# Kernel tuning notes

Measured on AMD Instinct MI355X. Metric: run time of the kernel, lower is better.

## Reference

```python
import jax, jax.numpy as jnp
import numpy as np


def setup_inputs() -> dict:
    key = jax.random.key(0)
    kq, kk, kv = jax.random.split(key, 3)
    B, S, D = 32, 2048, 64
    q = jax.random.normal(kq, (B, S, D), dtype=jnp.float32)
    k = jax.random.normal(kk, (B, S, D), dtype=jnp.float32)
    v = jax.random.normal(kv, (B, S, D), dtype=jnp.float32)
    return {"q": q, "k": k, "v": v}


def reference(q, k, v):
    # attention = q @ k^T  -> [B, S, S]; scale=None, attn_mask=None path
    scores = jnp.einsum("bqd,bkd->bqk", q, k)
    attention = jax.nn.softmax(scores, axis=-1)  # softmax over dim=2 (last)
    # dropout p=0.0 -> identity
    context = jnp.einsum("bqk,bkd->bqd", attention, v) + q  # residual add
    return (context, attention)
```

## Files before the change

### kernel.cpp

```cpp
#include <hip/hip_runtime.h>

namespace {

constexpr int kB = 32;
constexpr int kS = 2048;
constexpr int kD = 64;
constexpr int BQ = 128;
constexpr int BK = 64;
constexpr int LW = 72;
constexpr int NT = kS / BK;
constexpr int NP = NT / 2;
constexpr int KSZ = BK * LW;
constexpr float kLog2e = 1.44269504088896340736f;

typedef _Float16 f16x8 __attribute__((ext_vector_type(8)));
typedef _Float16 f16x4 __attribute__((ext_vector_type(4)));
typedef float f32x4 __attribute__((ext_vector_type(4)));

#define MFMA16F(a, b, c) __builtin_amdgcn_mfma_f32_16x16x32_f16(a, b, c, 0, 0, 0)

#define LBAR()                                                  \
    do {                                                        \
        asm volatile("s_waitcnt lgkmcnt(0)" ::: "memory");      \
        __builtin_amdgcn_s_barrier();                           \
        asm volatile("" ::: "memory");                          \
    } while (0)

__global__ __launch_bounds__(512, 4)
void sdpa_kernel(const float* __restrict__ qg, const float* __restrict__ kg,
                 const float* __restrict__ vg, float* __restrict__ out) {
    __shared__ _Float16 smem[4 * KSZ + 8 * 16 * LW];
    _Float16* sP = smem + 4 * KSZ;
    _Float16* sQ = smem;

    const int tid = threadIdx.x;
    const int lane = tid & 63;
    const int g = lane >> 4;
    const int c = lane & 15;
    const int wq = tid >> 6;
    const int wrow0 = wq * 16;

    const int id = blockIdx.x;
    const int lin = (id & 7) * 64 + (id >> 3);
    const int b = lin >> 4;
    const int q0 = (lin & 15) * BQ;

    float* ctx = out;
    float* att = out + (size_t)kB * kS * kD;
    const size_t inb = (size_t)b * kS * kD;
    const float* kbase = kg + inb;

    const int srow = tid >> 4;
    const int scol = (tid & 15) * 4;

    const int vd = lane;
    const int j0v = wq * 8;

    f32x4 kr[2][2];
    #pragma unroll
    for (int t = 0; t < 2; ++t)
        #pragma unroll
        for (int i = 0; i < 2; ++i)
            kr[t][i] = *reinterpret_cast<const f32x4*>(
                kbase + (size_t)(t * BK + i * 32 + srow) * kD + scol);

    #pragma unroll
    for (int i = 0; i < 4; ++i) {
        const int row = i * 32 + srow;
        f32x4 qv = *reinterpret_cast<const f32x4*>(qg + inb + (size_t)(q0 + row) * kD + scol);
        f16x4 hv;
        #pragma unroll
        for (int e = 0; e < 4; ++e) hv[e] = (_Float16)(qv[e] * kLog2e);
        *reinterpret_cast<f16x4*>(&sQ[row * LW + scol]) = hv;
    }
    LBAR();
    f16x8 aQ0 = *reinterpret_cast<const f16x8*>(&sQ[(wrow0 + c) * LW + 8 * g]);
    f16x8 aQ1 = *reinterpret_cast<const f16x8*>(&sQ[(wrow0 + c) * LW + 32 + 8 * g]);
    LBAR();

    #pragma unroll
    for (int t = 0; t < 2; ++t)
        #pragma unroll
        for (int i = 0; i < 2; ++i) {
            const int row = i * 32 + srow;
            f16x4 hv;
            #pragma unroll
            for (int e = 0; e < 4; ++e) hv[e] = (_Float16)kr[t][i][e];
            *reinterpret_cast<f16x4*>(&smem[t * KSZ + row * LW + scol]) = hv;
        }
    #pragma unroll
    for (int t = 0; t < 2; ++t)
        #pragma unroll
        for (int i = 0; i < 2; ++i)
            kr[t][i] = *reinterpret_cast<const f32x4*>(
                kbase + (size_t)((2 + t) * BK + i * 32 + srow) * kD + scol);
    LBAR();

    float l_l = 0.f;

    for (int pt = 0; pt < NP; ++pt) {
        const _Float16* bcur = smem + (pt & 1) * 2 * KSZ;
        _Float16* bnxt = smem + ((pt + 1) & 1) * 2 * KSZ;
        if (pt + 1 < NP) {
            #pragma unroll
            for (int t = 0; t < 2; ++t)
                #pragma unroll
                for (int i = 0; i < 2; ++i) {
                    const int row = i * 32 + srow;
                    f16x4 hv;
                    #pragma unroll
                    for (int e = 0; e < 4; ++e) hv[e] = (_Float16)kr[t][i][e];
                    *reinterpret_cast<f16x4*>(&bnxt[t * KSZ + row * LW + scol]) = hv;
                }
        }
        if (pt + 2 < NP) {
            #pragma unroll
            for (int t = 0; t < 2; ++t)
                #pragma unroll
                for (int i = 0; i < 2; ++i)
                    kr[t][i] = *reinterpret_cast<const f32x4*>(
                        kbase + (size_t)(((pt + 2) * 2 + t) * BK + i * 32 + srow) * kD + scol);
        }
        __builtin_amdgcn_s_setprio(1);
        #pragma unroll
        for (int t = 0; t < 2; ++t) {
            const _Float16* sKc = bcur + t * KSZ;
            #pragma unroll
            for (int ct = 0; ct < 4; ++ct) {
                const int jc = 16 * ct + c;
                f16x8 b0 = *reinterpret_cast<const f16x8*>(&sKc[jc * LW + 8 * g]);
                f16x8 b1 = *reinterpret_cast<const f16x8*>(&sKc[jc * LW + 32 + 8 * g]);
                f32x4 s = {0.f, 0.f, 0.f, 0.f};
                s = MFMA16F(b0, aQ0, s);
                s = MFMA16F(b1, aQ1, s);
                #pragma unroll
                for (int r = 0; r < 4; ++r)
                    l_l += __builtin_amdgcn_exp2f(s[r]);
            }
        }
        __builtin_amdgcn_s_setprio(0);
        if (pt + 1 < NP) LBAR();
    }

    f32x4 kr2[2];
    float vr[8];
    #pragma unroll
    for (int i = 0; i < 2; ++i)
        kr2[i] = *reinterpret_cast<const f32x4*>(kbase + (size_t)(i * 32 + srow) * kD + scol);
    #pragma unroll
    for (int e = 0; e < 8; ++e)
        vr[e] = vg[inb + (size_t)(j0v + e) * kD + vd];

    l_l += __shfl_xor(l_l, 16);
    l_l += __shfl_xor(l_l, 32);
    const float dexp = -__builtin_amdgcn_logf(l_l);

    f32x4 accpv[4];
    #pragma unroll
    for (int dt = 0; dt < 4; ++dt) accpv[dt] = {0.f, 0.f, 0.f, 0.f};

    _Float16* myP = sP + wq * 16 * LW;

    LBAR();
    #pragma unroll
    for (int i = 0; i < 2; ++i) {
        const int row = i * 32 + srow;
        f16x4 hv;
        #pragma unroll
        for (int e = 0; e < 4; ++e) hv[e] = (_Float16)kr2[i][e];
        *reinterpret_cast<f16x4*>(&smem[row * LW + scol]) = hv;
    }
    {
        f16x8 vv;
        #pragma unroll
        for (int e = 0; e < 8; ++e) vv[e] = (_Float16)vr[e];
        *reinterpret_cast<f16x8*>(&smem[2 * KSZ + vd * LW + j0v]) = vv;
    }
    #pragma unroll
    for (int i = 0; i < 2; ++i)
        kr2[i] = *reinterpret_cast<const f32x4*>(kbase + (size_t)(BK + i * 32 + srow) * kD + scol);
    #pragma unroll
    for (int e = 0; e < 8; ++e)
        vr[e] = vg[inb + (size_t)(BK + j0v + e) * kD + vd];
    LBAR();

    for (int kt = 0; kt < NT; ++kt) {
        const int j0 = kt * BK;
        const _Float16* sKc = smem + (kt & 1) * KSZ;
        const _Float16* sVc = smem + 2 * KSZ + (kt & 1) * KSZ;
        _Float16* sKn = smem + ((kt + 1) & 1) * KSZ;
        _Float16* sVn = smem + 2 * KSZ + ((kt + 1) & 1) * KSZ;
        if (kt + 1 < NT) {
            #pragma unroll
            for (int i = 0; i < 2; ++i) {
                const int row = i * 32 + srow;
                f16x4 hv;
                #pragma unroll
                for (int e = 0; e < 4; ++e) hv[e] = (_Float16)kr2[i][e];
                *reinterpret_cast<f16x4*>(&sKn[row * LW + scol]) = hv;
            }
            f16x8 vv;
            #pragma unroll
            for (int e = 0; e < 8; ++e) vv[e] = (_Float16)vr[e];
            *reinterpret_cast<f16x8*>(&sVn[vd * LW + j0v]) = vv;
        }
        if (kt + 2 < NT) {
            const int j0n = (kt + 2) * BK;
            #pragma unroll
            for (int i = 0; i < 2; ++i)
                kr2[i] = *reinterpret_cast<const f32x4*>(kbase + (size_t)(j0n + i * 32 + srow) * kD + scol);
            #pragma unroll
            for (int e = 0; e < 8; ++e)
                vr[e] = vg[inb + (size_t)(j0n + j0v + e) * kD + vd];
        }
        __builtin_amdgcn_s_setprio(1);
        #pragma unroll
        for (int ct = 0; ct < 4; ++ct) {
            const int jc = 16 * ct + c;
            f16x8 b0 = *reinterpret_cast<const f16x8*>(&sKc[jc * LW + 8 * g]);
            f16x8 b1 = *reinterpret_cast<const f16x8*>(&sKc[jc * LW + 32 + 8 * g]);
            f32x4 s = {dexp, dexp, dexp, dexp};
            s = MFMA16F(b0, aQ0, s);
            s = MFMA16F(b1, aQ1, s);
            f32x4 po;
            f16x4 pv;
            #pragma unroll
            for (int r = 0; r < 4; ++r) {
                const float p = __builtin_amdgcn_exp2f(s[r]);
                po[r] = p;
                pv[r] = (_Float16)p;
            }
            *reinterpret_cast<f32x4*>(
                att + ((size_t)b * kS + (size_t)(q0 + wrow0 + c)) * kS + j0 + 16 * ct + 4 * g) = po;
            *reinterpret_cast<f16x4*>(&myP[c * LW + 16 * ct + 4 * g]) = pv;
        }
        f16x8 aP0 = *reinterpret_cast<const f16x8*>(&myP[c * LW + 8 * g]);
        f16x8 aP1 = *reinterpret_cast<const f16x8*>(&myP[c * LW + 32 + 8 * g]);
        #pragma unroll
        for (int dt = 0; dt < 4; ++dt) {
            f16x8 bv0 = *reinterpret_cast<const f16x8*>(&sVc[(16 * dt + c) * LW + 8 * g]);
            f16x8 bv1 = *reinterpret_cast<const f16x8*>(&sVc[(16 * dt + c) * LW + 32 + 8 * g]);
            accpv[dt] = MFMA16F(aP0, bv0, accpv[dt]);
            accpv[dt] = MFMA16F(aP1, bv1, accpv[dt]);
        }
        __builtin_amdgcn_s_setprio(0);
        if (kt + 1 < NT) LBAR();
    }

    #pragma unroll
    for (int dt = 0; dt < 4; ++dt) {
        #pragma unroll
        for (int r = 0; r < 4; ++r) {
            const size_t rowg = (size_t)b * kS + (size_t)(q0 + wrow0 + 4 * g + r);
            const int d = 16 * dt + c;
            ctx[rowg * kD + d] = accpv[dt][r] + qg[rowg * kD + d];
        }
    }
}

}

extern "C" void kernel_launch(void* const* d_in, const int* in_sizes, int n_in,
                              void* d_out, int out_size, void* d_ws, size_t ws_size,
                              hipStream_t stream) {
    const float* q = (const float*)d_in[0];
    const float* k = (const float*)d_in[1];
    const float* v = (const float*)d_in[2];
    float* out = (float*)d_out;
    dim3 grid(kB * (kS / BQ));
    dim3 block(512);
    hipLaunchKernelGGL(sdpa_kernel, grid, block, 0, stream, q, k, v, out);
}
```

Measured before the change: 186.8 us.

## Load K directly into registers for row-sum pass and use nontemporal output stores

The first pass, which computes softmax row sums, no longer stages K tiles through double-buffered shared memory with barriers. Each wave now loads its MFMA operand fragments of K straight from global memory into registers, prefetching the next tile while converting the current one. This drops the LDS writes and barriers from that pass, but every wave re-reads K from global memory or cache instead of sharing it across the block. The attention and context outputs are also written with nontemporal stores to limit cache pollution.

```diff
diff --git a/kernel.cpp b/kernel.cpp
--- a/kernel.cpp
+++ b/kernel.cpp
@@ -9,7 +9,6 @@
 constexpr int BK = 64;
 constexpr int LW = 72;
 constexpr int NT = kS / BK;
-constexpr int NP = NT / 2;
 constexpr int KSZ = BK * LW;
 constexpr float kLog2e = 1.44269504088896340736f;
 
@@ -56,13 +55,15 @@
     const int vd = lane;
     const int j0v = wq * 8;
 
-    f32x4 kr[2][2];
-    #pragma unroll
-    for (int t = 0; t < 2; ++t)
-        #pragma unroll
-        for (int i = 0; i < 2; ++i)
-            kr[t][i] = *reinterpret_cast<const f32x4*>(
-                kbase + (size_t)(t * BK + i * 32 + srow) * kD + scol);
+    f32x4 kw[16];
+    #pragma unroll
+    for (int ct = 0; ct < 4; ++ct) {
+        const float* kp = kbase + (size_t)(16 * ct + c) * kD + 8 * g;
+        kw[4 * ct + 0] = *reinterpret_cast<const f32x4*>(kp);
+        kw[4 * ct + 1] = *reinterpret_cast<const f32x4*>(kp + 4);
+        kw[4 * ct + 2] = *reinterpret_cast<const f32x4*>(kp + 32);
+        kw[4 * ct + 3] = *reinterpret_cast<const f32x4*>(kp + 36);
+    }
 
     #pragma unroll
     for (int i = 0; i < 4; ++i) {
@@ -78,68 +79,32 @@
     f16x8 aQ1 = *reinterpret_cast<const f16x8*>(&sQ[(wrow0 + c) * LW + 32 + 8 * g]);
     LBAR();
 
-    #pragma unroll
-    for (int t = 0; t < 2; ++t)
-        #pragma unroll
-        for (int i = 0; i < 2; ++i) {
-            const int row = i * 32 + srow;
-            f16x4 hv;
-            #pragma unroll
-            for (int e = 0; e < 4; ++e) hv[e] = (_Float16)kr[t][i][e];
-            *reinterpret_cast<f16x4*>(&smem[t * KSZ + row * LW + scol]) = hv;
-        }
-    #pragma unroll
-    for (int t = 0; t < 2; ++t)
-        #pragma unroll
-        for (int i = 0; i < 2; ++i)
-            kr[t][i] = *reinterpret_cast<const f32x4*>(
-                kbase + (size_t)((2 + t) * BK + i * 32 + srow) * kD + scol);
-    LBAR();
-
     float l_l = 0.f;
 
-    for (int pt = 0; pt < NP; ++pt) {
-        const _Float16* bcur = smem + (pt & 1) * 2 * KSZ;
-        _Float16* bnxt = smem + ((pt + 1) & 1) * 2 * KSZ;
-        if (pt + 1 < NP) {
-            #pragma unroll
-            for (int t = 0; t < 2; ++t)
-                #pragma unroll
-                for (int i = 0; i < 2; ++i) {
-                    const int row = i * 32 + srow;
-                    f16x4 hv;
-                    #pragma unroll
-                    for (int e = 0; e < 4; ++e) hv[e] = (_Float16)kr[t][i][e];
-                    *reinterpret_cast<f16x4*>(&bnxt[t * KSZ + row * LW + scol]) = hv;
-                }
-        }
-        if (pt + 2 < NP) {
-            #pragma unroll
-            for (int t = 0; t < 2; ++t)
-                #pragma unroll
-                for (int i = 0; i < 2; ++i)
-                    kr[t][i] = *reinterpret_cast<const f32x4*>(
-                        kbase + (size_t)(((pt + 2) * 2 + t) * BK + i * 32 + srow) * kD + scol);
-        }
-        __builtin_amdgcn_s_setprio(1);
-        #pragma unroll
-        for (int t = 0; t < 2; ++t) {
-            const _Float16* sKc = bcur + t * KSZ;
-            #pragma unroll
-            for (int ct = 0; ct < 4; ++ct) {
-                const int jc = 16 * ct + c;
-                f16x8 b0 = *reinterpret_cast<const f16x8*>(&sKc[jc * LW + 8 * g]);
-                f16x8 b1 = *reinterpret_cast<const f16x8*>(&sKc[jc * LW + 32 + 8 * g]);
-                f32x4 s = {0.f, 0.f, 0.f, 0.f};
-                s = MFMA16F(b0, aQ0, s);
-                s = MFMA16F(b1, aQ1, s);
-                #pragma unroll
-                for (int r = 0; r < 4; ++r)
-                    l_l += __builtin_amdgcn_exp2f(s[r]);
+    for (int kt = 0; kt < NT; ++kt) {
+        const int jn = (kt + 1 < NT) ? (kt + 1) * BK : 0;
+        #pragma unroll
+        for (int ct = 0; ct < 4; ++ct) {
+            f16x8 b0, b1;
+            #pragma unroll
+            for (int e = 0; e < 4; ++e) {
+                b0[e]     = (_Float16)kw[4 * ct + 0][e];
+                b0[4 + e] = (_Float16)kw[4 * ct + 1][e];
+                b1[e]     = (_Float16)kw[4 * ct + 2][e];
+                b1[4 + e] = (_Float16)kw[4 * ct + 3][e];
             }
-        }
-        __builtin_amdgcn_s_setprio(0);
-        if (pt + 1 < NP) LBAR();
+            const float* kp = kbase + (size_t)(jn + 16 * ct + c) * kD + 8 * g;
+            kw[4 * ct + 0] = *reinterpret_cast<const f32x4*>(kp);
+            kw[4 * ct + 1] = *reinterpret_cast<const f32x4*>(kp + 4);
+            kw[4 * ct + 2] = *reinterpret_cast<const f32x4*>(kp + 32);
+            kw[4 * ct + 3] = *reinterpret_cast<const f32x4*>(kp + 36);
+            f32x4 s = {0.f, 0.f, 0.f, 0.f};
+            s = MFMA16F(b0, aQ0, s);
+            s = MFMA16F(b1, aQ1, s);
+            #pragma unroll
+            for (int r = 0; r < 4; ++r)
+                l_l += __builtin_amdgcn_exp2f(s[r]);
+        }
     }
 
     f32x4 kr2[2];
@@ -161,7 +126,6 @@
 
     _Float16* myP = sP + wq * 16 * LW;
 
-    LBAR();
     #pragma unroll
     for (int i = 0; i < 2; ++i) {
         const int row = i * 32 + srow;
@@ -230,8 +194,8 @@
                 po[r] = p;
                 pv[r] = (_Float16)p;
             }
-            *reinterpret_cast<f32x4*>(
-                att + ((size_t)b * kS + (size_t)(q0 + wrow0 + c)) * kS + j0 + 16 * ct + 4 * g) = po;
+            __builtin_nontemporal_store(po, reinterpret_cast<f32x4*>(
+                att + ((size_t)b * kS + (size_t)(q0 + wrow0 + c)) * kS + j0 + 16 * ct + 4 * g));
             *reinterpret_cast<f16x4*>(&myP[c * LW + 16 * ct + 4 * g]) = pv;
         }
         f16x8 aP0 = *reinterpret_cast<const f16x8*>(&myP[c * LW + 8 * g]);
@@ -253,7 +217,8 @@
         for (int r = 0; r < 4; ++r) {
             const size_t rowg = (size_t)b * kS + (size_t)(q0 + wrow0 + 4 * g + r);
             const int d = 16 * dt + c;
-            ctx[rowg * kD + d] = accpv[dt][r] + qg[rowg * kD + d];
+            __builtin_nontemporal_store(accpv[dt][r] + qg[rowg * kD + d],
+                                        ctx + rowg * kD + d);
         }
     }
 }
```

New measurement: 342.6 us. 83.4% more time.
